# Kernel tuning notes

Measured on AMD Instinct MI355X. Metric: run time of the kernel, lower is better.

Reference implementation:

```python
import jax, jax.numpy as jnp
import numpy as np

D_MODEL = 256
N_HEADS = 4
D_FF = 1024
N = 6144
N_DOMS = 1024
LN_EPS = 1e-5
NEG_INF = -1e30


def setup_inputs() -> dict:
    key = jax.random.key(0)
    ks = jax.random.split(key, 10)
    x = jax.random.normal(ks[0], (N, D_MODEL), dtype=jnp.float32)
    pulse_to_dom_idx = jnp.sort(jax.random.randint(ks[1], (N,), 0, N_DOMS, dtype=jnp.int32))
    s = 0.02
    return {
        "x": x,
        "pulse_to_dom_idx": pulse_to_dom_idx,
        "qkv_w": jax.random.normal(ks[2], (D_MODEL, 3 * D_MODEL), dtype=jnp.float32) * s,
        "qkv_b": jnp.zeros((3 * D_MODEL,), dtype=jnp.float32),
        "out_w": jax.random.normal(ks[3], (D_MODEL, D_MODEL), dtype=jnp.float32) * s,
        "out_b": jnp.zeros((D_MODEL,), dtype=jnp.float32),
        "ff_w1": jax.random.normal(ks[4], (D_MODEL, D_FF), dtype=jnp.float32) * s,
        "ff_b1": jnp.zeros((D_FF,), dtype=jnp.float32),
        "ff_w2": jax.random.normal(ks[5], (D_FF, D_MODEL), dtype=jnp.float32) * s,
        "ff_b2": jnp.zeros((D_MODEL,), dtype=jnp.float32),
        "ln1_g": jnp.ones((D_MODEL,), dtype=jnp.float32),
        "ln1_b": jnp.zeros((D_MODEL,), dtype=jnp.float32),
        "ln2_g": jnp.ones((D_MODEL,), dtype=jnp.float32),
        "ln2_b": jnp.zeros((D_MODEL,), dtype=jnp.float32),
    }


def _layer_norm(x, g, b):
    mu = jnp.mean(x, axis=-1, keepdims=True)
    var = jnp.mean(jnp.square(x - mu), axis=-1, keepdims=True)
    return (x - mu) * jax.lax.rsqrt(var + LN_EPS) * g + b


def reference(x, pulse_to_dom_idx, qkv_w, qkv_b, out_w, out_b,
              ff_w1, ff_b1, ff_w2, ff_b2, ln1_g, ln1_b, ln2_g, ln2_b):
    n, d = x.shape
    hd = d // N_HEADS
    # --- document-masked multi-head attention (dense, matching FlexAttention score_mod) ---
    qkv = x @ qkv_w + qkv_b                      # (N, 3D)
    q, k, v = jnp.split(qkv, 3, axis=-1)
    q = q.reshape(n, N_HEADS, hd)
    k = k.reshape(n, N_HEADS, hd)
    v = v.reshape(n, N_HEADS, hd)
    scores = jnp.einsum('qhd,khd->hqk', q, k) / jnp.sqrt(jnp.float32(hd))  # (H, N, N)
    same_doc = pulse_to_dom_idx[:, None] == pulse_to_dom_idx[None, :]      # (N, N)
    scores = jnp.where(same_doc[None], scores, NEG_INF)
    attn = jax.nn.softmax(scores, axis=-1)
    attn_out = jnp.einsum('hqk,khd->qhd', attn, v).reshape(n, d)
    attn_out = attn_out @ out_w + out_b
    # --- residual + norm + FFN + residual + norm (dropout in eval mode) ---
    x = _layer_norm(x + attn_out, ln1_g, ln1_b)
    ff = jax.nn.gelu(x @ ff_w1 + ff_b1, approximate=False) @ ff_w2 + ff_b2
    x = _layer_norm(x + ff, ln2_g, ln2_b)
    return x
```

## Files before the change

kernel.cpp:

```cpp
#include <hip/hip_runtime.h>
#include <hip/hip_bf16.h>
#include <math.h>

constexpr int NP  = 6144;
constexpr int DM  = 256;
constexpr int DFF = 1024;
constexpr float LNEPS = 1e-5f;

typedef __attribute__((ext_vector_type(8))) short short8;
typedef __attribute__((ext_vector_type(4))) short short4v;
typedef __attribute__((ext_vector_type(4))) float f32x4;

__device__ __forceinline__ short f2bf(float f) {
    unsigned u = __builtin_bit_cast(unsigned, f);
    unsigned r = u + 0x7FFFu + ((u >> 16) & 1u);
    return (short)(r >> 16);
}
__device__ __forceinline__ float bf2f(short s) {
    unsigned u = ((unsigned)(unsigned short)s) << 16;
    return __builtin_bit_cast(float, u);
}

#define GLOAD16(gp, lp)                                                        \
    __builtin_amdgcn_global_load_lds(                                          \
        (const __attribute__((address_space(1))) unsigned int*)(gp),           \
        (__attribute__((address_space(3))) unsigned int*)(lp), 16, 0, 0)

__device__ __forceinline__ int lds_idx(int row, int chunk) {
    return row * 64 + ((chunk ^ (row & 7)) * 8);
}
__device__ __forceinline__ int lds_idx128(int row, int chunk) {
    return row * 128 + ((chunk ^ (row & 7)) * 8);
}

__global__ __launch_bounds__(256) void prep_kernel(
    const float* __restrict__ qkv_w, const float* __restrict__ out_w,
    const float* __restrict__ ff_w1, const float* __restrict__ ff_w2,
    short* __restrict__ qkvT, short* __restrict__ outT,
    short* __restrict__ ff1T, short* __restrict__ ff2T,
    const int* __restrict__ dom, int* __restrict__ seg_s,
    int* __restrict__ seg_e, const float* __restrict__ x,
    short* __restrict__ xB) {
    int b = blockIdx.x;
    if (b >= 792) {
        int i = (b - 792) * 2048 + threadIdx.x * 8;
        float4 a0 = *(const float4*)&x[i];
        float4 a1 = *(const float4*)&x[i + 4];
        short8 v = { f2bf(a0.x), f2bf(a0.y), f2bf(a0.z), f2bf(a0.w),
                     f2bf(a1.x), f2bf(a1.y), f2bf(a1.z), f2bf(a1.w) };
        *(short8*)&xB[i] = v;
        return;
    }
    if (b >= 768) {
        int i = (b - 768) * 256 + threadIdx.x;
        if (i >= NP) return;
        int d = dom[i];
        int s = i;
        while (s > 0 && dom[s - 1] == d) --s;
        int e = i + 1;
        while (e < NP && dom[e] == d) ++e;
        seg_s[i] = s;
        seg_e[i] = e;
        return;
    }
    const float* src;
    short* dst;
    int K, Nn;
    if (b < 192)      { src = qkv_w; dst = qkvT; K = 256;  Nn = 768; }
    else if (b < 256) { b -= 192; src = out_w; dst = outT; K = 256;  Nn = 256; }
    else if (b < 512) { b -= 256; src = ff_w1; dst = ff1T; K = 256;  Nn = 1024; }
    else              { b -= 512; src = ff_w2; dst = ff2T; K = 1024; Nn = 256; }
    int tpr = Nn / 32;
    int k0 = (b / tpr) * 32, n0 = (b % tpr) * 32;

    __shared__ float lds[32][36];
    int t = threadIdx.x;
    {
        int k = t >> 3, n = (t & 7) * 4;
        *(float4*)&lds[k][n] = *(const float4*)&src[(size_t)(k0 + k) * Nn + n0 + n];
    }
    __syncthreads();
    {
        int n = t >> 3, ks = (t & 7) * 4;
        short4v o = { f2bf(lds[ks + 0][n]), f2bf(lds[ks + 1][n]),
                      f2bf(lds[ks + 2][n]), f2bf(lds[ks + 3][n]) };
        *(short4v*)&dst[(size_t)(n0 + n) * K + k0 + ks] = o;
    }
}

template <int EPI>
__global__ __launch_bounds__(256) void mgemm128x64(
    const short* __restrict__ A, const short* __restrict__ Bt,
    const float* __restrict__ bias, short* __restrict__ C, int Nn, int K) {
    __shared__ __align__(16) short As[128 * 128];
    __shared__ __align__(16) short Bs[64 * 128];

    const int tid = threadIdx.x, lane = tid & 63, w = tid >> 6;
    const int wm = (w >> 1) * 64, wn = (w & 1) * 32;

    const int nx = gridDim.x;
    const int bid = blockIdx.y * nx + blockIdx.x;
    const int q = (nx * gridDim.y) >> 3;
    const int id2 = (bid & 7) * q + (bid >> 3);
    const int rowBase = (id2 / nx) * 128, colBase = (id2 % nx) * 64;

    const int lr4 = lane >> 4;
    const int c16 = lane & 15;
    const int fr = lane & 15, g4 = lane >> 4;

    f32x4 acc[4][2];
#pragma unroll
    for (int i = 0; i < 4; ++i)
#pragma unroll
        for (int j = 0; j < 2; ++j) acc[i][j] = f32x4{0.f, 0.f, 0.f, 0.f};

    for (int k0 = 0; k0 < K; k0 += 128) {
#pragma unroll
        for (int i = 0; i < 12; ++i) {
            int g = w * 12 + i;
            if (g < 32) {
                int row = g * 4 + lr4;
                int sc = c16 ^ (row & 7);
                GLOAD16(A + (size_t)(rowBase + row) * K + k0 + sc * 8, &As[g * 512]);
            } else {
                int row = (g - 32) * 4 + lr4;
                int sc = c16 ^ (row & 7);
                GLOAD16(Bt + (size_t)(colBase + row) * K + k0 + sc * 8,
                        &Bs[(g - 32) * 512]);
            }
        }
        __syncthreads();

#pragma unroll
        for (int kk = 0; kk < 4; ++kk) {
            int j = kk * 4 + g4;
            short8 af[4], bfv[2];
#pragma unroll
            for (int f = 0; f < 4; ++f)
                af[f] = *(const short8*)&As[lds_idx128(wm + f * 16 + fr, j)];
#pragma unroll
            for (int f = 0; f < 2; ++f)
                bfv[f] = *(const short8*)&Bs[lds_idx128(wn + f * 16 + fr, j)];
#pragma unroll
            for (int fm = 0; fm < 4; ++fm)
#pragma unroll
                for (int fn = 0; fn < 2; ++fn)
                    acc[fm][fn] = __builtin_amdgcn_mfma_f32_16x16x32_bf16(
                        af[fm], bfv[fn], acc[fm][fn], 0, 0, 0);
        }
        __syncthreads();
    }

    const int cr = g4 * 4;
#pragma unroll
    for (int fm = 0; fm < 4; ++fm)
#pragma unroll
        for (int fn = 0; fn < 2; ++fn) {
            int c = colBase + wn + fn * 16 + fr;
            float bv = bias[c];
#pragma unroll
            for (int j = 0; j < 4; ++j) {
                int r = rowBase + wm + fm * 16 + cr + j;
                float v = acc[fm][fn][j] + bv;
                if (EPI == 1) v = 0.5f * v * (1.0f + erff(v * 0.70710678118654752f));
                C[(size_t)r * Nn + c] = f2bf(v);
            }
        }
}

template <int EPI>
__global__ __launch_bounds__(256) void mgemm64(
    const short* __restrict__ A, const short* __restrict__ Bt,
    const float* __restrict__ bias, const short* __restrict__ res,
    void* __restrict__ Cv, int Nn, int K) {
    __shared__ __align__(16) short As[64 * 128];
    __shared__ __align__(16) short Bs[64 * 128];

    const int tid = threadIdx.x, lane = tid & 63, w = tid >> 6;
    const int wm = (w >> 1) * 32, wn = (w & 1) * 32;

    const int nx = gridDim.x;
    const int bid = blockIdx.y * nx + blockIdx.x;
    const int q = (nx * gridDim.y) >> 3;
    const int id2 = (bid & 7) * q + (bid >> 3);
    const int rowBase = (id2 / nx) * 64, colBase = (id2 % nx) * 64;

    const int lr4 = lane >> 4;
    const int c16 = lane & 15;
    const int fr = lane & 15, g4 = lane >> 4;

    f32x4 acc[2][2];
#pragma unroll
    for (int i = 0; i < 2; ++i)
#pragma unroll
        for (int j = 0; j < 2; ++j) acc[i][j] = f32x4{0.f, 0.f, 0.f, 0.f};

    for (int k0 = 0; k0 < K; k0 += 128) {
#pragma unroll
        for (int i = 0; i < 4; ++i) {
            int g = w * 4 + i;
            int row = g * 4 + lr4;
            int sc = c16 ^ (row & 7);
            GLOAD16(A  + (size_t)(rowBase + row) * K + k0 + sc * 8, &As[g * 512]);
            GLOAD16(Bt + (size_t)(colBase + row) * K + k0 + sc * 8, &Bs[g * 512]);
        }
        __syncthreads();

#pragma unroll
        for (int kk = 0; kk < 4; ++kk) {
            int j = kk * 4 + g4;
            short8 af[2], bfv[2];
#pragma unroll
            for (int f = 0; f < 2; ++f) {
                af[f]  = *(const short8*)&As[lds_idx128(wm + f * 16 + fr, j)];
                bfv[f] = *(const short8*)&Bs[lds_idx128(wn + f * 16 + fr, j)];
            }
#pragma unroll
            for (int fm = 0; fm < 2; ++fm)
#pragma unroll
                for (int fn = 0; fn < 2; ++fn)
                    acc[fm][fn] = __builtin_amdgcn_mfma_f32_16x16x32_bf16(
                        af[fm], bfv[fn], acc[fm][fn], 0, 0, 0);
        }
        __syncthreads();
    }

    const int cr = g4 * 4;
#pragma unroll
    for (int fm = 0; fm < 2; ++fm)
#pragma unroll
        for (int fn = 0; fn < 2; ++fn) {
            int c = colBase + wn + fn * 16 + fr;
            float bv = bias[c];
#pragma unroll
            for (int j = 0; j < 4; ++j) {
                int r = rowBase + wm + fm * 16 + cr + j;
                float v = acc[fm][fn][j] + bv;
                if (EPI == 1) v = 0.5f * v * (1.0f + erff(v * 0.70710678118654752f));
                if (EPI == 2)
                    ((float*)Cv)[(size_t)r * Nn + c] =
                        v + bf2f(res[(size_t)r * 256 + c]);
                else
                    ((short*)Cv)[(size_t)r * Nn + c] = f2bf(v);
            }
        }
}

__global__ __launch_bounds__(256) void ln_kernel(
    const float* __restrict__ in, const float* __restrict__ g,
    const float* __restrict__ b, float* __restrict__ out) {
    int wid = blockIdx.x * 4 + (threadIdx.x >> 6);
    int lane = threadIdx.x & 63;

    float4 v = ((const float4*)(in + (size_t)wid * 256))[lane];
    float s = v.x + v.y + v.z + v.w;
#pragma unroll
    for (int off = 32; off; off >>= 1) s += __shfl_xor(s, off);
    float mu = s * (1.0f / 256.0f);
    float dx = v.x - mu, dy = v.y - mu, dz = v.z - mu, dw = v.w - mu;
    float ss = dx * dx + dy * dy + dz * dz + dw * dw;
#pragma unroll
    for (int off = 32; off; off >>= 1) ss += __shfl_xor(ss, off);
    float rstd = rsqrtf(ss * (1.0f / 256.0f) + LNEPS);

    float4 gg = ((const float4*)g)[lane];
    float4 bb = ((const float4*)b)[lane];
    float4 o;
    o.x = dx * rstd * gg.x + bb.x;
    o.y = dy * rstd * gg.y + bb.y;
    o.z = dz * rstd * gg.z + bb.z;
    o.w = dw * rstd * gg.w + bb.w;
    ((float4*)(out + (size_t)wid * 256))[lane] = o;
}

__global__ __launch_bounds__(512) void attnln_kernel(
    const short* __restrict__ qkvB, const int* __restrict__ seg_s,
    const int* __restrict__ seg_e, const short* __restrict__ outT,
    const float* __restrict__ out_b, const float* __restrict__ xres,
    const float* __restrict__ gw, const float* __restrict__ bw,
    short* __restrict__ x1) {
    __shared__ __align__(16) short As[16 * 256];
    __shared__ __align__(16) short Bs[256 * 128];
    __shared__ float r1[8][16], r2[8][16];

    const int tid = threadIdx.x, lane = tid & 63, w = tid >> 6;
    const int rowBase = blockIdx.x * 16;
    const int lr4 = lane >> 4, c16 = lane & 15;
    const int fr = lane & 15, g4 = lane >> 4;

    {
        const int l8 = lane & 7;
        const int G  = (w << 3) | (lane >> 3);
        int r = G >> 2, h = G & 3;
        int row = rowBase + r;
        short8 qv = *(const short8*)&qkvB[(size_t)row * 768 + h * 64 + l8 * 8];
        float qd[8];
#pragma unroll
        for (int e = 0; e < 8; ++e) qd[e] = bf2f(qv[e]);
        int ss = seg_s[row], ee = seg_e[row];
        float m = -INFINITY, l = 0.0f;
        float acc[8] = {0.f, 0.f, 0.f, 0.f, 0.f, 0.f, 0.f, 0.f};
        for (int j = ss; j < ee; ++j) {
            short8 kv = *(const short8*)&qkvB[(size_t)j * 768 + 256 + h * 64 + l8 * 8];
            short8 vv = *(const short8*)&qkvB[(size_t)j * 768 + 512 + h * 64 + l8 * 8];
            float prod = 0.f;
#pragma unroll
            for (int e = 0; e < 8; ++e) prod += qd[e] * bf2f(kv[e]);
            prod += __shfl_xor(prod, 1);
            prod += __shfl_xor(prod, 2);
            prod += __shfl_xor(prod, 4);
            float score = prod * 0.125f;
            float mn = fmaxf(m, score);
            float scale = __expf(m - mn);
            float p = __expf(score - mn);
            l = l * scale + p;
#pragma unroll
            for (int e = 0; e < 8; ++e) acc[e] = acc[e] * scale + p * bf2f(vv[e]);
            m = mn;
        }
        float inv = 1.0f / l;
        int c = h * 8 + l8;
        short8 o;
#pragma unroll
        for (int e = 0; e < 8; ++e) o[e] = f2bf(acc[e] * inv);
        *(short8*)&As[r * 256 + ((c ^ (r & 7)) * 8)] = o;
    }
    __syncthreads();

    f32x4 acc[2];
    acc[0] = f32x4{0.f, 0.f, 0.f, 0.f};
    acc[1] = f32x4{0.f, 0.f, 0.f, 0.f};

    for (int k0 = 0; k0 < 256; k0 += 128) {
#pragma unroll
        for (int i = 0; i < 8; ++i) {
            int g = w * 8 + i;
            int row = g * 4 + lr4;
            int sc = c16 ^ (row & 7);
            GLOAD16(outT + (size_t)row * 256 + k0 + sc * 8, &Bs[g * 512]);
        }
        __syncthreads();
#pragma unroll
        for (int kk = 0; kk < 4; ++kk) {
            int j = kk * 4 + g4;
            int cj = (k0 >> 3) + j;
            short8 af = *(const short8*)&As[fr * 256 + ((cj ^ (fr & 7)) * 8)];
            short8 bfv[2];
#pragma unroll
            for (int fn = 0; fn < 2; ++fn)
                bfv[fn] = *(const short8*)&Bs[lds_idx128(w * 32 + fn * 16 + fr, j)];
#pragma unroll
            for (int fn = 0; fn < 2; ++fn)
                acc[fn] = __builtin_amdgcn_mfma_f32_16x16x32_bf16(
                    af, bfv[fn], acc[fn], 0, 0, 0);
        }
        __syncthreads();
    }

    float v[2][4], p1[4], p2[4];
#pragma unroll
    for (int j = 0; j < 4; ++j) { p1[j] = 0.f; p2[j] = 0.f; }
#pragma unroll
    for (int fn = 0; fn < 2; ++fn) {
        int c = w * 32 + fn * 16 + fr;
        float bv = out_b[c];
#pragma unroll
        for (int j = 0; j < 4; ++j) {
            int r = rowBase + g4 * 4 + j;
            float t = acc[fn][j] + bv + xres[(size_t)r * 256 + c];
            v[fn][j] = t;
            p1[j] += t;
            p2[j] += t * t;
        }
    }
#pragma unroll
    for (int m = 1; m < 16; m <<= 1)
#pragma unroll
        for (int j = 0; j < 4; ++j) {
            p1[j] += __shfl_xor(p1[j], m);
            p2[j] += __shfl_xor(p2[j], m);
        }
    if (fr == 0) {
#pragma unroll
        for (int j = 0; j < 4; ++j) {
            r1[w][g4 * 4 + j] = p1[j];
            r2[w][g4 * 4 + j] = p2[j];
        }
    }
    __syncthreads();
#pragma unroll
    for (int j = 0; j < 4; ++j) {
        int rl = g4 * 4 + j;
        int r = rowBase + rl;
        float s1 = 0.f, s2 = 0.f;
#pragma unroll
        for (int ww = 0; ww < 8; ++ww) { s1 += r1[ww][rl]; s2 += r2[ww][rl]; }
        float mu = s1 * (1.0f / 256.0f);
        float var = s2 * (1.0f / 256.0f) - mu * mu;
        float rstd = rsqrtf(var + LNEPS);
#pragma unroll
        for (int fn = 0; fn < 2; ++fn) {
            int c = w * 32 + fn * 16 + fr;
            float o = (v[fn][j] - mu) * rstd * gw[c] + bw[c];
            x1[(size_t)r * 256 + c] = f2bf(o);
        }
    }
}

extern "C" void kernel_launch(void* const* d_in, const int* in_sizes, int n_in,
                              void* d_out, int out_size, void* d_ws, size_t ws_size,
                              hipStream_t stream) {
    const float* x      = (const float*)d_in[0];
    const int*   dom    = (const int*)d_in[1];
    const float* qkv_w  = (const float*)d_in[2];
    const float* qkv_b  = (const float*)d_in[3];
    const float* out_w  = (const float*)d_in[4];
    const float* out_b  = (const float*)d_in[5];
    const float* ff_w1  = (const float*)d_in[6];
    const float* ff_b1  = (const float*)d_in[7];
    const float* ff_w2  = (const float*)d_in[8];
    const float* ff_b2  = (const float*)d_in[9];
    const float* ln1_g  = (const float*)d_in[10];
    const float* ln1_b  = (const float*)d_in[11];
    const float* ln2_g  = (const float*)d_in[12];
    const float* ln2_b  = (const float*)d_in[13];
    float* out = (float*)d_out;

    short* xB     = (short*)d_ws;
    short* qkvB   = xB + (size_t)NP * 256;
    short* x1     = qkvB + (size_t)NP * 768;
    short* hB     = x1 + (size_t)NP * 256;
    short* qkvT   = hB + (size_t)NP * 1024;
    short* outT   = qkvT + 768 * 256;
    short* ff1T   = outT + 256 * 256;
    short* ff2T   = ff1T + 1024 * 256;
    int* seg_s    = (int*)(ff2T + 256 * 1024);
    int* seg_e    = seg_s + NP;
    float* y      = (float*)(seg_e + NP);

    prep_kernel<<<1560, 256, 0, stream>>>(qkv_w, out_w, ff_w1, ff_w2,
                                          qkvT, outT, ff1T, ff2T,
                                          dom, seg_s, seg_e, x, xB);

    mgemm128x64<0><<<dim3(768 / 64, NP / 128), 256, 0, stream>>>(
        xB, qkvT, qkv_b, qkvB, 768, 256);

    attnln_kernel<<<NP / 16, 512, 0, stream>>>(
        qkvB, seg_s, seg_e, outT, out_b, x, ln1_g, ln1_b, x1);

    mgemm128x64<1><<<dim3(DFF / 64, NP / 128), 256, 0, stream>>>(
        x1, ff1T, ff_b1, hB, 1024, 256);

    mgemm64<2><<<dim3(DM / 64, NP / 64), 256, 0, stream>>>(
        hB, ff2T, ff_b2, x1, y, 256, 1024);

    ln_kernel<<<NP / 4, 256, 0, stream>>>(y, ln2_g, ln2_b, out);
}
```

Baseline: 59.67 us.

## Fuse FF2 GEMM with residual add and final LayerNorm into one kernel

Replaces the 64x64-tiled FF2 GEMM and the separate LayerNorm kernel with one 16-row-by-256-column kernel that computes the full output row, adds bias and the residual, and applies LayerNorm in the epilogue. This removes the fp32 intermediate write and re-read plus one launch. The cost is that each block reloads the entire 256x1024 weight slice and reuses it for only 16 rows, raising L2 traffic, and the variance is now computed as E[x^2]-mu^2 in one pass. It also raises wave priority around the MFMA loop in the attention/out-projection kernel.

```diff
diff --git a/kernel.cpp b/kernel.cpp
--- a/kernel.cpp
+++ b/kernel.cpp
@@ -168,109 +168,101 @@
         }
 }
 
-template <int EPI>
-__global__ __launch_bounds__(256) void mgemm64(
+__global__ __launch_bounds__(512) void gemmln16(
     const short* __restrict__ A, const short* __restrict__ Bt,
     const float* __restrict__ bias, const short* __restrict__ res,
-    void* __restrict__ Cv, int Nn, int K) {
-    __shared__ __align__(16) short As[64 * 128];
-    __shared__ __align__(16) short Bs[64 * 128];
+    const float* __restrict__ gw, const float* __restrict__ bw,
+    float* __restrict__ out) {
+    __shared__ __align__(16) short As[16 * 128];
+    __shared__ __align__(16) short Bs[256 * 128];
+    __shared__ float r1[8][16], r2[8][16];
 
     const int tid = threadIdx.x, lane = tid & 63, w = tid >> 6;
-    const int wm = (w >> 1) * 32, wn = (w & 1) * 32;
-
-    const int nx = gridDim.x;
-    const int bid = blockIdx.y * nx + blockIdx.x;
-    const int q = (nx * gridDim.y) >> 3;
-    const int id2 = (bid & 7) * q + (bid >> 3);
-    const int rowBase = (id2 / nx) * 64, colBase = (id2 % nx) * 64;
-
-    const int lr4 = lane >> 4;
-    const int c16 = lane & 15;
+    const int rowBase = blockIdx.x * 16;
+    const int lr4 = lane >> 4, c16 = lane & 15;
     const int fr = lane & 15, g4 = lane >> 4;
 
-    f32x4 acc[2][2];
-#pragma unroll
-    for (int i = 0; i < 2; ++i)
-#pragma unroll
-        for (int j = 0; j < 2; ++j) acc[i][j] = f32x4{0.f, 0.f, 0.f, 0.f};
-
-    for (int k0 = 0; k0 < K; k0 += 128) {
-#pragma unroll
-        for (int i = 0; i < 4; ++i) {
-            int g = w * 4 + i;
+    f32x4 acc[2];
+    acc[0] = f32x4{0.f, 0.f, 0.f, 0.f};
+    acc[1] = f32x4{0.f, 0.f, 0.f, 0.f};
+
+    for (int k0 = 0; k0 < 1024; k0 += 128) {
+        if (w < 4) {
+            int row = w * 4 + lr4;
+            int sc = c16 ^ (row & 7);
+            GLOAD16(A + (size_t)(rowBase + row) * 1024 + k0 + sc * 8, &As[w * 512]);
+        }
+#pragma unroll
+        for (int i = 0; i < 8; ++i) {
+            int g = w * 8 + i;
             int row = g * 4 + lr4;
             int sc = c16 ^ (row & 7);
-            GLOAD16(A  + (size_t)(rowBase + row) * K + k0 + sc * 8, &As[g * 512]);
-            GLOAD16(Bt + (size_t)(colBase + row) * K + k0 + sc * 8, &Bs[g * 512]);
-        }
-        __syncthreads();
-
+            GLOAD16(Bt + (size_t)row * 1024 + k0 + sc * 8, &Bs[g * 512]);
+        }
+        __syncthreads();
 #pragma unroll
         for (int kk = 0; kk < 4; ++kk) {
             int j = kk * 4 + g4;
-            short8 af[2], bfv[2];
-#pragma unroll
-            for (int f = 0; f < 2; ++f) {
-                af[f]  = *(const short8*)&As[lds_idx128(wm + f * 16 + fr, j)];
-                bfv[f] = *(const short8*)&Bs[lds_idx128(wn + f * 16 + fr, j)];
-            }
-#pragma unroll
-            for (int fm = 0; fm < 2; ++fm)
-#pragma unroll
-                for (int fn = 0; fn < 2; ++fn)
-                    acc[fm][fn] = __builtin_amdgcn_mfma_f32_16x16x32_bf16(
-                        af[fm], bfv[fn], acc[fm][fn], 0, 0, 0);
-        }
-        __syncthreads();
-    }
-
-    const int cr = g4 * 4;
-#pragma unroll
-    for (int fm = 0; fm < 2; ++fm)
+            short8 af = *(const short8*)&As[lds_idx128(fr, j)];
+            short8 bfv[2];
+#pragma unroll
+            for (int fn = 0; fn < 2; ++fn)
+                bfv[fn] = *(const short8*)&Bs[lds_idx128(w * 32 + fn * 16 + fr, j)];
+#pragma unroll
+            for (int fn = 0; fn < 2; ++fn)
+                acc[fn] = __builtin_amdgcn_mfma_f32_16x16x32_bf16(
+                    af, bfv[fn], acc[fn], 0, 0, 0);
+        }
+        __syncthreads();
+    }
+
+    float v[2][4], p1[4], p2[4];
+#pragma unroll
+    for (int j = 0; j < 4; ++j) { p1[j] = 0.f; p2[j] = 0.f; }
+#pragma unroll
+    for (int fn = 0; fn < 2; ++fn) {
+        int c = w * 32 + fn * 16 + fr;
+        float bv = bias[c];
+#pragma unroll
+        for (int j = 0; j < 4; ++j) {
+            int r = rowBase + g4 * 4 + j;
+            float t = acc[fn][j] + bv + bf2f(res[(size_t)r * 256 + c]);
+            v[fn][j] = t;
+            p1[j] += t;
+            p2[j] += t * t;
+        }
+    }
+#pragma unroll
+    for (int m = 1; m < 16; m <<= 1)
+#pragma unroll
+        for (int j = 0; j < 4; ++j) {
+            p1[j] += __shfl_xor(p1[j], m);
+            p2[j] += __shfl_xor(p2[j], m);
+        }
+    if (fr == 0) {
+#pragma unroll
+        for (int j = 0; j < 4; ++j) {
+            r1[w][g4 * 4 + j] = p1[j];
+            r2[w][g4 * 4 + j] = p2[j];
+        }
+    }
+    __syncthreads();
+#pragma unroll
+    for (int j = 0; j < 4; ++j) {
+        int rl = g4 * 4 + j;
+        int r = rowBase + rl;
+        float s1 = 0.f, s2 = 0.f;
+#pragma unroll
+        for (int ww = 0; ww < 8; ++ww) { s1 += r1[ww][rl]; s2 += r2[ww][rl]; }
+        float mu = s1 * (1.0f / 256.0f);
+        float var = s2 * (1.0f / 256.0f) - mu * mu;
+        float rstd = rsqrtf(var + LNEPS);
 #pragma unroll
         for (int fn = 0; fn < 2; ++fn) {
-            int c = colBase + wn + fn * 16 + fr;
-            float bv = bias[c];
-#pragma unroll
-            for (int j = 0; j < 4; ++j) {
-                int r = rowBase + wm + fm * 16 + cr + j;
-                float v = acc[fm][fn][j] + bv;
-                if (EPI == 1) v = 0.5f * v * (1.0f + erff(v * 0.70710678118654752f));
-                if (EPI == 2)
-                    ((float*)Cv)[(size_t)r * Nn + c] =
-                        v + bf2f(res[(size_t)r * 256 + c]);
-                else
-                    ((short*)Cv)[(size_t)r * Nn + c] = f2bf(v);
-            }
-        }
-}
-
-__global__ __launch_bounds__(256) void ln_kernel(
-    const float* __restrict__ in, const float* __restrict__ g,
-    const float* __restrict__ b, float* __restrict__ out) {
-    int wid = blockIdx.x * 4 + (threadIdx.x >> 6);
-    int lane = threadIdx.x & 63;
-
-    float4 v = ((const float4*)(in + (size_t)wid * 256))[lane];
-    float s = v.x + v.y + v.z + v.w;
-#pragma unroll
-    for (int off = 32; off; off >>= 1) s += __shfl_xor(s, off);
-    float mu = s * (1.0f / 256.0f);
-    float dx = v.x - mu, dy = v.y - mu, dz = v.z - mu, dw = v.w - mu;
-    float ss = dx * dx + dy * dy + dz * dz + dw * dw;
-#pragma unroll
-    for (int off = 32; off; off >>= 1) ss += __shfl_xor(ss, off);
-    float rstd = rsqrtf(ss * (1.0f / 256.0f) + LNEPS);
-
-    float4 gg = ((const float4*)g)[lane];
-    float4 bb = ((const float4*)b)[lane];
-    float4 o;
-    o.x = dx * rstd * gg.x + bb.x;
-    o.y = dy * rstd * gg.y + bb.y;
-    o.z = dz * rstd * gg.z + bb.z;
-    o.w = dw * rstd * gg.w + bb.w;
-    ((float4*)(out + (size_t)wid * 256))[lane] = o;
+            int c = w * 32 + fn * 16 + fr;
+            out[(size_t)r * 256 + c] = (v[fn][j] - mu) * rstd * gw[c] + bw[c];
+        }
+    }
 }
 
 __global__ __launch_bounds__(512) void attnln_kernel(
@@ -340,6 +332,7 @@
             GLOAD16(outT + (size_t)row * 256 + k0 + sc * 8, &Bs[g * 512]);
         }
         __syncthreads();
+        __builtin_amdgcn_s_setprio(1);
 #pragma unroll
         for (int kk = 0; kk < 4; ++kk) {
             int j = kk * 4 + g4;
@@ -354,6 +347,7 @@
                 acc[fn] = __builtin_amdgcn_mfma_f32_16x16x32_bf16(
                     af, bfv[fn], acc[fn], 0, 0, 0);
         }
+        __builtin_amdgcn_s_setprio(0);
         __syncthreads();
     }
 
@@ -436,7 +430,6 @@
     short* ff2T   = ff1T + 1024 * 256;
     int* seg_s    = (int*)(ff2T + 256 * 1024);
     int* seg_e    = seg_s + NP;
-    float* y      = (float*)(seg_e + NP);
 
     prep_kernel<<<1560, 256, 0, stream>>>(qkv_w, out_w, ff_w1, ff_w2,
                                           qkvT, outT, ff1T, ff2T,
@@ -451,8 +444,6 @@
     mgemm128x64<1><<<dim3(DFF / 64, NP / 128), 256, 0, stream>>>(
         x1, ff1T, ff_b1, hB, 1024, 256);
 
-    mgemm64<2><<<dim3(DM / 64, NP / 64), 256, 0, stream>>>(
-        hB, ff2T, ff_b2, x1, y, 256, 1024);
-
-    ln_kernel<<<NP / 4, 256, 0, stream>>>(y, ln2_g, ln2_b, out);
-}
+    gemmln16<<<NP / 16, 512, 0, stream>>>(
+        hB, ff2T, ff_b2, x1, ln2_g, ln2_b, out);
+}
```

Result: slower. 61.95 us (+3.8%).
